# Kernel optimization log

Measured on AMD Instinct MI355X. Metric: run time of the kernel, lower is better.

## Reference

```python
import jax, jax.numpy as jnp
import numpy as np

N_NODES = 50000
N_EDGES = 800000
D_IN = 512
LATENT = [512, 512, 512]
L2_EPS = 1e-12  # torch F.normalize clamp_min


def _gin_layer(x, src, dst, W, b, eps):
    # sum aggregation of neighbor (source) features into destination nodes
    agg = jax.ops.segment_sum(x[src], dst, num_segments=x.shape[0])  # [N, d]
    h = agg + (1.0 + eps) * x
    return jax.nn.relu(h @ W + b)  # Sequential(Linear, ReLU)


def _l2_normalize(x):
    n = jnp.sqrt(jnp.sum(x * x, axis=-1, keepdims=True))
    return x / jnp.maximum(n, L2_EPS)


def setup_inputs() -> dict:
    key = jax.random.key(0)
    ks = jax.random.split(key, 10)
    x = jax.random.normal(ks[0], (N_NODES, D_IN), dtype=jnp.float32)
    edge_index = jax.random.randint(ks[1], (2, N_EDGES), 0, N_NODES, dtype=jnp.int32)
    dims = [D_IN] + LATENT
    inp = {"x": x, "edge_index": edge_index}
    for i in range(3):
        fan_in = dims[i]
        bound = 1.0 / np.sqrt(fan_in)
        inp[f"W{i+1}"] = jax.random.uniform(ks[2 + 2 * i], (dims[i], dims[i + 1]), jnp.float32, -bound, bound)
        inp[f"b{i+1}"] = jax.random.uniform(ks[3 + 2 * i], (dims[i + 1],), jnp.float32, -bound, bound)
        inp[f"eps{i+1}"] = jnp.zeros((), dtype=jnp.float32)  # train_eps=True, init 0
    return inp


def reference(x, edge_index, W1, b1, eps1, W2, b2, eps2, W3, b3, eps3):
    src, dst = edge_index[0], edge_index[1]
    # layers 0..num_layers-2: GINConv -> L2 normalize -> ReLU
    h = _gin_layer(x, src, dst, W1, b1, eps1)
    h = jax.nn.relu(_l2_normalize(h))
    h = _gin_layer(h, src, dst, W2, b2, eps2)
    h = jax.nn.relu(_l2_normalize(h))
    # final layer: raw GINConv output = logits
    logits = _gin_layer(h, src, dst, W3, b3, eps3)
    probs = jax.nn.softmax(logits, axis=-1)
    return (logits, probs)
```

## Files before the change

### kernel.cpp

```cpp
#include <hip/hip_runtime.h>
#include <stdint.h>

#define N_NODES 50000
#define N_EDGES 800000

typedef unsigned int uint32;

__device__ inline float bflo(uint32 u) { return __builtin_bit_cast(float, u << 16); }
__device__ inline float bfhi(uint32 u) { return __builtin_bit_cast(float, u & 0xffff0000u); }
__device__ inline float bf2f(unsigned short h) { return __builtin_bit_cast(float, (uint32)h << 16); }
__device__ inline unsigned short f2bf(float f) {
    uint32 u = __builtin_bit_cast(uint32, f);
    u += 0x7fffu + ((u >> 16) & 1u);
    return (unsigned short)(u >> 16);
}
__device__ inline uint32 pack2(float lo, float hi) {
    return (uint32)f2bf(lo) | ((uint32)f2bf(hi) << 16);
}

__global__ __launch_bounds__(256) void zero_k(int* p, int n) {
    int i = blockIdx.x * 256 + threadIdx.x;
    if (i < n) p[i] = 0;
}

__global__ __launch_bounds__(256) void count_k(const int* __restrict__ ei, int* __restrict__ cnt) {
    int e = blockIdx.x * 256 + threadIdx.x;
    if (e < N_EDGES) atomicAdd(&cnt[ei[N_EDGES + e]], 1);
}

#define NB 196

__global__ __launch_bounds__(256) void blocksum_k(const int* __restrict__ cnt, int* __restrict__ bsum) {
    int i = blockIdx.x * 256 + threadIdx.x;
    int v = (i < N_NODES) ? cnt[i] : 0;
#pragma unroll
    for (int off = 32; off > 0; off >>= 1) v += __shfl_down(v, off);
    __shared__ int sh[4];
    int w = threadIdx.x >> 6, lane = threadIdx.x & 63;
    if (lane == 0) sh[w] = v;
    __syncthreads();
    if (threadIdx.x == 0) bsum[blockIdx.x] = sh[0] + sh[1] + sh[2] + sh[3];
}

__global__ __launch_bounds__(256) void bscan_k(const int* __restrict__ bsum, int* __restrict__ bpre,
                                               int* __restrict__ rowptr) {
    __shared__ int sh[256];
    int t = threadIdx.x;
    int v = (t < NB) ? bsum[t] : 0;
    sh[t] = v;
    __syncthreads();
    for (int d = 1; d < 256; d <<= 1) {
        int u = (t >= d) ? sh[t - d] : 0;
        __syncthreads();
        sh[t] += u;
        __syncthreads();
    }
    if (t < NB) bpre[t] = sh[t] - v;
    if (t == NB - 1) rowptr[N_NODES] = sh[t];
}

__global__ __launch_bounds__(256) void scatter_k(int* __restrict__ cnt, const int* __restrict__ bpre,
                                                 int* __restrict__ rowptr) {
    int b = blockIdx.x, t = threadIdx.x, i = b * 256 + t;
    int w = t >> 6, lane = t & 63;
    int myv = (i < N_NODES) ? cnt[i] : 0;
    int v = myv;
#pragma unroll
    for (int d = 1; d < 64; d <<= 1) {
        int u = __shfl_up(v, d);
        if (lane >= d) v += u;
    }
    __shared__ int wt[4];
    if (lane == 63) wt[w] = v;
    __syncthreads();
    int off = bpre[b];
    for (int k = 0; k < w; k++) off += wt[k];
    int excl = v - myv + off;
    if (i < N_NODES) {
        rowptr[i] = excl;
        cnt[i] = excl;
    }
}

__global__ __launch_bounds__(256) void fill_k(const int* __restrict__ ei, int* __restrict__ cursor,
                                              int* __restrict__ csr) {
    int e = blockIdx.x * 256 + threadIdx.x;
    if (e < N_EDGES) {
        int d = ei[N_EDGES + e];
        int p = atomicAdd(&cursor[d], 1);
        csr[p] = ei[e];
    }
}

__global__ __launch_bounds__(256) void wprep_k(const float* __restrict__ W,
                                               unsigned short* __restrict__ Whi,
                                               unsigned short* __restrict__ Wlo) {
    __shared__ float sh[64][65];
    int bk = (blockIdx.x & 7) * 64;
    int bn = (blockIdx.x >> 3) * 64;
    int t = threadIdx.x;
    int lr = t >> 4;
    int lc4 = (t & 15) * 4;
#pragma unroll
    for (int i = 0; i < 4; i++) {
        int k = lr + i * 16;
        float4 v = *(const float4*)&W[(size_t)(bk + k) * 512 + bn + lc4];
        sh[k][lc4] = v.x; sh[k][lc4 + 1] = v.y; sh[k][lc4 + 2] = v.z; sh[k][lc4 + 3] = v.w;
    }
    __syncthreads();
#pragma unroll
    for (int i = 0; i < 4; i++) {
        int n = lr + i * 16;
        float w0 = sh[lc4][n], w1 = sh[lc4 + 1][n], w2 = sh[lc4 + 2][n], w3 = sh[lc4 + 3][n];
        ushort4 h, l;
        h.x = f2bf(w0); l.x = f2bf(w0 - bf2f(h.x));
        h.y = f2bf(w1); l.y = f2bf(w1 - bf2f(h.y));
        h.z = f2bf(w2); l.z = f2bf(w2 - bf2f(h.z));
        h.w = f2bf(w3); l.w = f2bf(w3 - bf2f(h.w));
        *(ushort4*)&Whi[(size_t)(bn + n) * 512 + bk + lc4] = h;
        *(ushort4*)&Wlo[(size_t)(bn + n) * 512 + bk + lc4] = l;
    }
}

__global__ __launch_bounds__(256) void xconv_k(const float4* __restrict__ x, uint2* __restrict__ xb) {
    int i = blockIdx.x * 256 + threadIdx.x;
    float4 v = x[i];
    uint2 o;
    o.x = pack2(v.x, v.y);
    o.y = pack2(v.z, v.w);
    xb[i] = o;
}

__global__ __launch_bounds__(256) void scale_k(const uint4* __restrict__ in, const float* __restrict__ ss,
                                               uint4* __restrict__ outp) {
    int node = blockIdx.x * 4 + (threadIdx.x >> 6);
    int lane = threadIdx.x & 63;
    float inv = 1.0f / fmaxf(sqrtf(ss[node]), 1e-12f);
    uint4 q = in[(size_t)node * 64 + lane];
    uint4 o;
    o.x = pack2(bflo(q.x) * inv, bfhi(q.x) * inv);
    o.y = pack2(bflo(q.y) * inv, bfhi(q.y) * inv);
    o.z = pack2(bflo(q.z) * inv, bfhi(q.z) * inv);
    o.w = pack2(bflo(q.w) * inv, bfhi(q.w) * inv);
    outp[(size_t)node * 64 + lane] = o;
}

#define ACC8(Q)                                                     \
    a0 += bflo(Q.x); a1 += bfhi(Q.x); a2 += bflo(Q.y); a3 += bfhi(Q.y); \
    a4 += bflo(Q.z); a5 += bfhi(Q.z); a6 += bflo(Q.w); a7 += bfhi(Q.w);

__global__ __launch_bounds__(256) void agg_k(const uint4* __restrict__ xin,
                                             const int* __restrict__ rowptr,
                                             const int* __restrict__ csr,
                                             const float* __restrict__ eps,
                                             uint4* __restrict__ hout) {
    int node = blockIdx.x * 4 + (threadIdx.x >> 6);
    int lane = threadIdx.x & 63;
    int beg = rowptr[node], end = rowptr[node + 1];
    float a0 = 0.f, a1 = 0.f, a2 = 0.f, a3 = 0.f, a4 = 0.f, a5 = 0.f, a6 = 0.f, a7 = 0.f;
    int e = beg;
    for (; e + 8 <= end; e += 8) {
        int s0 = csr[e],     s1 = csr[e + 1], s2 = csr[e + 2], s3 = csr[e + 3];
        int s4 = csr[e + 4], s5 = csr[e + 5], s6 = csr[e + 6], s7 = csr[e + 7];
        uint4 q0 = xin[(size_t)s0 * 64 + lane];
        uint4 q1 = xin[(size_t)s1 * 64 + lane];
        uint4 q2 = xin[(size_t)s2 * 64 + lane];
        uint4 q3 = xin[(size_t)s3 * 64 + lane];
        uint4 q4 = xin[(size_t)s4 * 64 + lane];
        uint4 q5 = xin[(size_t)s5 * 64 + lane];
        uint4 q6 = xin[(size_t)s6 * 64 + lane];
        uint4 q7 = xin[(size_t)s7 * 64 + lane];
        ACC8(q0) ACC8(q1) ACC8(q2) ACC8(q3)
        ACC8(q4) ACC8(q5) ACC8(q6) ACC8(q7)
    }
    for (; e + 4 <= end; e += 4) {
        int s0 = csr[e], s1 = csr[e + 1], s2 = csr[e + 2], s3 = csr[e + 3];
        uint4 q0 = xin[(size_t)s0 * 64 + lane];
        uint4 q1 = xin[(size_t)s1 * 64 + lane];
        uint4 q2 = xin[(size_t)s2 * 64 + lane];
        uint4 q3 = xin[(size_t)s3 * 64 + lane];
        ACC8(q0) ACC8(q1) ACC8(q2) ACC8(q3)
    }
    for (; e < end; ++e) {
        int s0 = csr[e];
        uint4 q0 = xin[(size_t)s0 * 64 + lane];
        ACC8(q0)
    }
    uint4 qs = xin[(size_t)node * 64 + lane];
    float ws = 1.0f + eps[0];
    a0 = fmaf(ws, bflo(qs.x), a0); a1 = fmaf(ws, bfhi(qs.x), a1);
    a2 = fmaf(ws, bflo(qs.y), a2); a3 = fmaf(ws, bfhi(qs.y), a3);
    a4 = fmaf(ws, bflo(qs.z), a4); a5 = fmaf(ws, bfhi(qs.z), a5);
    a6 = fmaf(ws, bflo(qs.w), a6); a7 = fmaf(ws, bfhi(qs.w), a7);
    uint4 o;
    o.x = pack2(a0, a1);
    o.y = pack2(a2, a3);
    o.z = pack2(a4, a5);
    o.w = pack2(a6, a7);
    hout[(size_t)node * 64 + lane] = o;
}

typedef __bf16 bf16x8 __attribute__((ext_vector_type(8)));
typedef float f32x4 __attribute__((ext_vector_type(4)));

__device__ inline void async16(const void* g, void* l) {
    __builtin_amdgcn_global_load_lds((const __attribute__((address_space(1))) void*)g,
                                     (__attribute__((address_space(3))) void*)l, 16, 0, 0);
}

template <bool SPLIT, bool F32OUT, bool NORM>
__global__ __launch_bounds__(256) void gemm_k(const unsigned short* __restrict__ A,
                                              const unsigned short* __restrict__ Whi,
                                              const unsigned short* __restrict__ Wlo,
                                              const float* __restrict__ bias,
                                              unsigned short* __restrict__ outB,
                                              float* __restrict__ outF,
                                              float* __restrict__ ssOut, int M) {
    constexpr int K = 512, N = 512, BK = 32, TM = 128;
    __shared__ unsigned short lds_a[TM * BK];
    __shared__ unsigned short lds_bh[TM * BK];
    __shared__ unsigned short lds_bl[SPLIT ? TM * BK : 16];
    const int t = threadIdx.x;
    const int w = t >> 6, lane = t & 63;
    const int wrow = w >> 1, wcol = w & 1;

    const int nwg = gridDim.x;
    const int qd = nwg >> 3, rd = nwg & 7;
    const int xcd = blockIdx.x & 7, jj = blockIdx.x >> 3;
    const int wg = (xcd < rd ? xcd * (qd + 1) : rd * (qd + 1) + (xcd - rd) * qd) + jj;
    const int m0 = (wg >> 2) * TM;
    const int n0 = (wg & 3) * TM;

    int r0 = w * 16 + (lane >> 2), cc = (lane & 3) * 8;
    int r1 = 64 + r0;
    int am0 = m0 + r0; am0 = am0 < M ? am0 : M - 1;
    int am1 = m0 + r1; am1 = am1 < M ? am1 : M - 1;
    const unsigned short* ag0 = A + (size_t)am0 * K + cc;
    const unsigned short* ag1 = A + (size_t)am1 * K + cc;
    const unsigned short* bh0 = Whi + (size_t)(n0 + r0) * K + cc;
    const unsigned short* bh1 = Whi + (size_t)(n0 + r1) * K + cc;
    const unsigned short* bl0 = Wlo + (size_t)(n0 + r0) * K + cc;
    const unsigned short* bl1 = Wlo + (size_t)(n0 + r1) * K + cc;
    unsigned short* la0 = lds_a + w * 512;
    unsigned short* la1 = lds_a + 2048 + w * 512;
    unsigned short* lh0 = lds_bh + w * 512;
    unsigned short* lh1 = lds_bh + 2048 + w * 512;
    unsigned short* ll0 = lds_bl + w * 512;
    unsigned short* ll1 = lds_bl + 2048 + w * 512;

    f32x4 acc[4][4] = {};
    const int quad = lane >> 4, l15 = lane & 15;
    const int arow = wrow * 64 + l15;
    const int brow = wcol * 64 + l15;

    for (int k0 = 0; k0 < K; k0 += BK) {
        __syncthreads();
        async16(ag0 + k0, la0);
        async16(ag1 + k0, la1);
        async16(bh0 + k0, lh0);
        async16(bh1 + k0, lh1);
        if (SPLIT) {
            async16(bl0 + k0, ll0);
            async16(bl1 + k0, ll1);
        }
        __syncthreads();
        bf16x8 af[4], bh[4], bl[4];
#pragma unroll
        for (int i = 0; i < 4; i++)
            af[i] = *(const bf16x8*)&lds_a[(arow + i * 16) * BK + quad * 8];
#pragma unroll
        for (int j = 0; j < 4; j++)
            bh[j] = *(const bf16x8*)&lds_bh[(brow + j * 16) * BK + quad * 8];
        if (SPLIT) {
#pragma unroll
            for (int j = 0; j < 4; j++)
                bl[j] = *(const bf16x8*)&lds_bl[(brow + j * 16) * BK + quad * 8];
        }
#pragma unroll
        for (int i = 0; i < 4; i++)
#pragma unroll
            for (int j = 0; j < 4; j++) {
                acc[i][j] = __builtin_amdgcn_mfma_f32_16x16x32_bf16(af[i], bh[j], acc[i][j], 0, 0, 0);
                if (SPLIT)
                    acc[i][j] = __builtin_amdgcn_mfma_f32_16x16x32_bf16(af[i], bl[j], acc[i][j], 0, 0, 0);
            }
    }

#pragma unroll
    for (int i = 0; i < 4; i++) {
        int mbase = m0 + wrow * 64 + i * 16 + quad * 4;
        float rs[4] = {0.f, 0.f, 0.f, 0.f};
#pragma unroll
        for (int j = 0; j < 4; j++) {
            int n = n0 + wcol * 64 + j * 16 + l15;
            float bv = bias[n];
#pragma unroll
            for (int r = 0; r < 4; r++) {
                int m = mbase + r;
                if (m < M) {
                    float v = fmaxf(acc[i][j][r] + bv, 0.0f);
                    if (NORM) rs[r] += v * v;
                    if (F32OUT) outF[(size_t)m * N + n] = v;
                    else        outB[(size_t)m * N + n] = f2bf(v);
                }
            }
        }
        if (NORM) {
#pragma unroll
            for (int r = 0; r < 4; r++) {
                float s = rs[r];
                s += __shfl_xor(s, 1);
                s += __shfl_xor(s, 2);
                s += __shfl_xor(s, 4);
                s += __shfl_xor(s, 8);
                int m = mbase + r;
                if (l15 == 0 && m < M) atomicAdd(&ssOut[m], s);
            }
        }
    }
}

__global__ __launch_bounds__(256) void softmax_k(const float* __restrict__ logits,
                                                 float* __restrict__ probs) {
    int node = blockIdx.x * 4 + (threadIdx.x >> 6);
    int lane = threadIdx.x & 63;
    const float4* zp = (const float4*)(logits + (size_t)node * 512);
    float4 q0 = zp[lane * 2], q1 = zp[lane * 2 + 1];
    float f[8] = {q0.x, q0.y, q0.z, q0.w, q1.x, q1.y, q1.z, q1.w};
    float m = f[0];
#pragma unroll
    for (int i = 1; i < 8; i++) m = fmaxf(m, f[i]);
#pragma unroll
    for (int off = 32; off > 0; off >>= 1) m = fmaxf(m, __shfl_xor(m, off));
    float e[8], s = 0.f;
#pragma unroll
    for (int i = 0; i < 8; i++) { e[i] = __expf(f[i] - m); s += e[i]; }
#pragma unroll
    for (int off = 32; off > 0; off >>= 1) s += __shfl_xor(s, off);
    float inv = 1.0f / s;
    float4* pp = (float4*)(probs + (size_t)node * 512);
    pp[lane * 2]     = make_float4(e[0] * inv, e[1] * inv, e[2] * inv, e[3] * inv);
    pp[lane * 2 + 1] = make_float4(e[4] * inv, e[5] * inv, e[6] * inv, e[7] * inv);
}

extern "C" void kernel_launch(void* const* d_in, const int* in_sizes, int n_in,
                              void* d_out, int out_size, void* d_ws, size_t ws_size,
                              hipStream_t stream) {
    (void)in_sizes; (void)n_in; (void)out_size; (void)ws_size;
    const float* x = (const float*)d_in[0];
    const int* ei = (const int*)d_in[1];
    const float* W1 = (const float*)d_in[2];
    const float* b1 = (const float*)d_in[3];
    const float* e1 = (const float*)d_in[4];
    const float* W2 = (const float*)d_in[5];
    const float* b2 = (const float*)d_in[6];
    const float* e2 = (const float*)d_in[7];
    const float* W3 = (const float*)d_in[8];
    const float* b3 = (const float*)d_in[9];
    const float* e3 = (const float*)d_in[10];
    float* out = (float*)d_out;
    float* out_logits = out;
    float* out_probs = out + (size_t)N_NODES * 512;

    char* ws = (char*)d_ws;
    int* rowptr = (int*)ws;
    int* cursor = rowptr + 50048;
    int* csr = cursor + 50048;
    int* bsum = csr + N_EDGES;
    int* bpre = bsum + 256;
    float* ss = (float*)(bpre + 256);
    float* ss1 = ss;
    float* ss2 = ss + 50048;
    unsigned short* Wsp = (unsigned short*)(ss + 2 * 50048);
    unsigned short* f0 = Wsp + 3 * 524288;
    unsigned short* fA = f0 + (size_t)N_NODES * 512;
    unsigned short* f1 = fA + (size_t)N_NODES * 512;
    unsigned short* f2 = f1 + (size_t)N_NODES * 512;

    zero_k<<<196, 256, 0, stream>>>(cursor, N_NODES);
    zero_k<<<392, 256, 0, stream>>>((int*)ss, 2 * 50048);
    count_k<<<(N_EDGES + 255) / 256, 256, 0, stream>>>(ei, cursor);
    blocksum_k<<<NB, 256, 0, stream>>>(cursor, bsum);
    bscan_k<<<1, 256, 0, stream>>>(bsum, bpre, rowptr);
    scatter_k<<<NB, 256, 0, stream>>>(cursor, bpre, rowptr);
    fill_k<<<(N_EDGES + 255) / 256, 256, 0, stream>>>(ei, cursor, csr);

    wprep_k<<<64, 256, 0, stream>>>(W1, Wsp,           Wsp + 262144);
    wprep_k<<<64, 256, 0, stream>>>(W2, Wsp + 524288,  Wsp + 786432);
    wprep_k<<<64, 256, 0, stream>>>(W3, Wsp + 1048576, Wsp + 1310720);

    xconv_k<<<25000, 256, 0, stream>>>((const float4*)x, (uint2*)f0);

    const int GG = 4 * ((N_NODES + 127) / 128);

    agg_k<<<12500, 256, 0, stream>>>((const uint4*)f0, rowptr, csr, e1, (uint4*)fA);
    gemm_k<false, false, true><<<GG, 256, 0, stream>>>(fA, Wsp, Wsp + 262144, b1, f1, nullptr, ss1, N_NODES);
    scale_k<<<12500, 256, 0, stream>>>((const uint4*)f1, ss1, (uint4*)f2);
    agg_k<<<12500, 256, 0, stream>>>((const uint4*)f2, rowptr, csr, e2, (uint4*)fA);
    gemm_k<false, false, true><<<GG, 256, 0, stream>>>(fA, Wsp + 524288, Wsp + 786432, b2, f1, nullptr, ss2, N_NODES);
    scale_k<<<12500, 256, 0, stream>>>((const uint4*)f1, ss2, (uint4*)f2);
    agg_k<<<12500, 256, 0, stream>>>((const uint4*)f2, rowptr, csr, e3, (uint4*)fA);
    gemm_k<true, true, false><<<GG, 256, 0, stream>>>(fA, Wsp + 1048576, Wsp + 1310720, b3, nullptr, out_logits, nullptr, N_NODES);
    softmax_k<<<N_NODES / 4, 256, 0, stream>>>(out_logits, out_probs);
}
```

Baseline: 1.004 ms.

## Fold L2 normalization into aggregation and double-buffer GEMM LDS loads

The separate scale pass that rewrote normalized bf16 features is replaced by a tiny per-node inverse-norm kernel. Aggregation then weights each gathered neighbor row by its inverse norm, which removes a full read and write of the 50000x512 feature tensor per layer. The GEMM main loop is also double-buffered: the next K-slice is loaded asynchronously into a second LDS buffer while MFMAs run on the current one, with one barrier per iteration instead of two. The costs are an extra scalar gather per edge, a change in rounding since features are no longer re-rounded after scaling, doubled LDS usage, and a possible race because only a barrier guards the async LDS loads.

```diff
diff --git a/kernel.cpp b/kernel.cpp
--- a/kernel.cpp
+++ b/kernel.cpp
@@ -131,28 +131,23 @@
     xb[i] = o;
 }
 
-__global__ __launch_bounds__(256) void scale_k(const uint4* __restrict__ in, const float* __restrict__ ss,
-                                               uint4* __restrict__ outp) {
-    int node = blockIdx.x * 4 + (threadIdx.x >> 6);
-    int lane = threadIdx.x & 63;
-    float inv = 1.0f / fmaxf(sqrtf(ss[node]), 1e-12f);
-    uint4 q = in[(size_t)node * 64 + lane];
-    uint4 o;
-    o.x = pack2(bflo(q.x) * inv, bfhi(q.x) * inv);
-    o.y = pack2(bflo(q.y) * inv, bfhi(q.y) * inv);
-    o.z = pack2(bflo(q.z) * inv, bfhi(q.z) * inv);
-    o.w = pack2(bflo(q.w) * inv, bfhi(q.w) * inv);
-    outp[(size_t)node * 64 + lane] = o;
-}
-
-#define ACC8(Q)                                                     \
-    a0 += bflo(Q.x); a1 += bfhi(Q.x); a2 += bflo(Q.y); a3 += bfhi(Q.y); \
-    a4 += bflo(Q.z); a5 += bfhi(Q.z); a6 += bflo(Q.w); a7 += bfhi(Q.w);
-
+__global__ __launch_bounds__(256) void invn_k(const float* __restrict__ ss, float* __restrict__ invn) {
+    int i = blockIdx.x * 256 + threadIdx.x;
+    if (i < N_NODES) invn[i] = 1.0f / fmaxf(sqrtf(ss[i]), 1e-12f);
+}
+
+#define ACCW(Q, W)                                                            \
+    a0 = fmaf(W, bflo(Q.x), a0); a1 = fmaf(W, bfhi(Q.x), a1);                 \
+    a2 = fmaf(W, bflo(Q.y), a2); a3 = fmaf(W, bfhi(Q.y), a3);                 \
+    a4 = fmaf(W, bflo(Q.z), a4); a5 = fmaf(W, bfhi(Q.z), a5);                 \
+    a6 = fmaf(W, bflo(Q.w), a6); a7 = fmaf(W, bfhi(Q.w), a7);
+
+template <bool SCALED>
 __global__ __launch_bounds__(256) void agg_k(const uint4* __restrict__ xin,
                                              const int* __restrict__ rowptr,
                                              const int* __restrict__ csr,
                                              const float* __restrict__ eps,
+                                             const float* __restrict__ invn,
                                              uint4* __restrict__ hout) {
     int node = blockIdx.x * 4 + (threadIdx.x >> 6);
     int lane = threadIdx.x & 63;
@@ -170,28 +165,26 @@
         uint4 q5 = xin[(size_t)s5 * 64 + lane];
         uint4 q6 = xin[(size_t)s6 * 64 + lane];
         uint4 q7 = xin[(size_t)s7 * 64 + lane];
-        ACC8(q0) ACC8(q1) ACC8(q2) ACC8(q3)
-        ACC8(q4) ACC8(q5) ACC8(q6) ACC8(q7)
-    }
-    for (; e + 4 <= end; e += 4) {
-        int s0 = csr[e], s1 = csr[e + 1], s2 = csr[e + 2], s3 = csr[e + 3];
-        uint4 q0 = xin[(size_t)s0 * 64 + lane];
-        uint4 q1 = xin[(size_t)s1 * 64 + lane];
-        uint4 q2 = xin[(size_t)s2 * 64 + lane];
-        uint4 q3 = xin[(size_t)s3 * 64 + lane];
-        ACC8(q0) ACC8(q1) ACC8(q2) ACC8(q3)
+        float w0 = SCALED ? invn[s0] : 1.0f;
+        float w1 = SCALED ? invn[s1] : 1.0f;
+        float w2 = SCALED ? invn[s2] : 1.0f;
+        float w3 = SCALED ? invn[s3] : 1.0f;
+        float w4 = SCALED ? invn[s4] : 1.0f;
+        float w5 = SCALED ? invn[s5] : 1.0f;
+        float w6 = SCALED ? invn[s6] : 1.0f;
+        float w7 = SCALED ? invn[s7] : 1.0f;
+        ACCW(q0, w0) ACCW(q1, w1) ACCW(q2, w2) ACCW(q3, w3)
+        ACCW(q4, w4) ACCW(q5, w5) ACCW(q6, w6) ACCW(q7, w7)
     }
     for (; e < end; ++e) {
         int s0 = csr[e];
         uint4 q0 = xin[(size_t)s0 * 64 + lane];
-        ACC8(q0)
+        float w0 = SCALED ? invn[s0] : 1.0f;
+        ACCW(q0, w0)
     }
     uint4 qs = xin[(size_t)node * 64 + lane];
-    float ws = 1.0f + eps[0];
-    a0 = fmaf(ws, bflo(qs.x), a0); a1 = fmaf(ws, bfhi(qs.x), a1);
-    a2 = fmaf(ws, bflo(qs.y), a2); a3 = fmaf(ws, bfhi(qs.y), a3);
-    a4 = fmaf(ws, bflo(qs.z), a4); a5 = fmaf(ws, bfhi(qs.z), a5);
-    a6 = fmaf(ws, bflo(qs.w), a6); a7 = fmaf(ws, bfhi(qs.w), a7);
+    float wsf = (1.0f + eps[0]) * (SCALED ? invn[node] : 1.0f);
+    ACCW(qs, wsf)
     uint4 o;
     o.x = pack2(a0, a1);
     o.y = pack2(a2, a3);
@@ -216,10 +209,11 @@
                                               unsigned short* __restrict__ outB,
                                               float* __restrict__ outF,
                                               float* __restrict__ ssOut, int M) {
-    constexpr int K = 512, N = 512, BK = 32, TM = 128;
-    __shared__ unsigned short lds_a[TM * BK];
-    __shared__ unsigned short lds_bh[TM * BK];
-    __shared__ unsigned short lds_bl[SPLIT ? TM * BK : 16];
+    constexpr int K = 512, N = 512, BK = 32, TM = 128, NK = K / BK;
+    constexpr int BUF = TM * BK;
+    __shared__ unsigned short lds_a[2 * BUF];
+    __shared__ unsigned short lds_bh[2 * BUF];
+    __shared__ unsigned short lds_bl[SPLIT ? 2 * BUF : 16];
     const int t = threadIdx.x;
     const int w = t >> 6, lane = t & 63;
     const int wrow = w >> 1, wcol = w & 1;
@@ -241,50 +235,63 @@
     const unsigned short* bh1 = Whi + (size_t)(n0 + r1) * K + cc;
     const unsigned short* bl0 = Wlo + (size_t)(n0 + r0) * K + cc;
     const unsigned short* bl1 = Wlo + (size_t)(n0 + r1) * K + cc;
-    unsigned short* la0 = lds_a + w * 512;
-    unsigned short* la1 = lds_a + 2048 + w * 512;
-    unsigned short* lh0 = lds_bh + w * 512;
-    unsigned short* lh1 = lds_bh + 2048 + w * 512;
-    unsigned short* ll0 = lds_bl + w * 512;
-    unsigned short* ll1 = lds_bl + 2048 + w * 512;
+    const int wo = w * 512;
 
     f32x4 acc[4][4] = {};
     const int quad = lane >> 4, l15 = lane & 15;
     const int arow = wrow * 64 + l15;
     const int brow = wcol * 64 + l15;
 
-    for (int k0 = 0; k0 < K; k0 += BK) {
+    auto stage = [&](int k0, int buf) {
+        unsigned short* da = lds_a + buf * BUF + wo;
+        unsigned short* dh = lds_bh + buf * BUF + wo;
+        async16(ag0 + k0, da);
+        async16(ag1 + k0, da + 2048);
+        async16(bh0 + k0, dh);
+        async16(bh1 + k0, dh + 2048);
+        if (SPLIT) {
+            unsigned short* dl = lds_bl + buf * BUF + wo;
+            async16(bl0 + k0, dl);
+            async16(bl1 + k0, dl + 2048);
+        }
+    };
+
+    auto compute = [&](int buf) {
+        const unsigned short* ba = lds_a + buf * BUF;
+        const unsigned short* bb = lds_bh + buf * BUF;
+        bf16x8 af[4], bhf[4], blf[4];
+#pragma unroll
+        for (int i = 0; i < 4; i++)
+            af[i] = *(const bf16x8*)&ba[(arow + i * 16) * BK + quad * 8];
+#pragma unroll
+        for (int j = 0; j < 4; j++)
+            bhf[j] = *(const bf16x8*)&bb[(brow + j * 16) * BK + quad * 8];
+        if (SPLIT) {
+            const unsigned short* bl = lds_bl + buf * BUF;
+#pragma unroll
+            for (int j = 0; j < 4; j++)
+                blf[j] = *(const bf16x8*)&bl[(brow + j * 16) * BK + quad * 8];
+        }
+#pragma unroll
+        for (int i = 0; i < 4; i++)
+#pragma unroll
+            for (int j = 0; j < 4; j++) {
+                acc[i][j] = __builtin_amdgcn_mfma_f32_16x16x32_bf16(af[i], bhf[j], acc[i][j], 0, 0, 0);
+                if (SPLIT)
+                    acc[i][j] = __builtin_amdgcn_mfma_f32_16x16x32_bf16(af[i], blf[j], acc[i][j], 0, 0, 0);
+            }
+    };
+
+    stage(0, 0);
+    __syncthreads();
+    int cur = 0;
+    for (int ks = 0; ks < NK - 1; ++ks) {
+        stage((ks + 1) * BK, cur ^ 1);
+        compute(cur);
         __syncthreads();
-        async16(ag0 + k0, la0);
-        async16(ag1 + k0, la1);
-        async16(bh0 + k0, lh0);
-        async16(bh1 + k0, lh1);
-        if (SPLIT) {
-            async16(bl0 + k0, ll0);
-            async16(bl1 + k0, ll1);
-        }
-        __syncthreads();
-        bf16x8 af[4], bh[4], bl[4];
-#pragma unroll
-        for (int i = 0; i < 4; i++)
-            af[i] = *(const bf16x8*)&lds_a[(arow + i * 16) * BK + quad * 8];
-#pragma unroll
-        for (int j = 0; j < 4; j++)
-            bh[j] = *(const bf16x8*)&lds_bh[(brow + j * 16) * BK + quad * 8];
-        if (SPLIT) {
-#pragma unroll
-            for (int j = 0; j < 4; j++)
-                bl[j] = *(const bf16x8*)&lds_bl[(brow + j * 16) * BK + quad * 8];
-        }
-#pragma unroll
-        for (int i = 0; i < 4; i++)
-#pragma unroll
-            for (int j = 0; j < 4; j++) {
-                acc[i][j] = __builtin_amdgcn_mfma_f32_16x16x32_bf16(af[i], bh[j], acc[i][j], 0, 0, 0);
-                if (SPLIT)
-                    acc[i][j] = __builtin_amdgcn_mfma_f32_16x16x32_bf16(af[i], bl[j], acc[i][j], 0, 0, 0);
-            }
-    }
+        cur ^= 1;
+    }
+    compute(cur);
 
 #pragma unroll
     for (int i = 0; i < 4; i++) {
@@ -368,14 +375,14 @@
     int* csr = cursor + 50048;
     int* bsum = csr + N_EDGES;
     int* bpre = bsum + 256;
-    float* ss = (float*)(bpre + 256);
+    float* invn = (float*)(bpre + 256);
+    float* ss = invn + 50048;
     float* ss1 = ss;
     float* ss2 = ss + 50048;
     unsigned short* Wsp = (unsigned short*)(ss + 2 * 50048);
     unsigned short* f0 = Wsp + 3 * 524288;
     unsigned short* fA = f0 + (size_t)N_NODES * 512;
     unsigned short* f1 = fA + (size_t)N_NODES * 512;
-    unsigned short* f2 = f1 + (size_t)N_NODES * 512;
 
     zero_k<<<196, 256, 0, stream>>>(cursor, N_NODES);
     zero_k<<<392, 256, 0, stream>>>((int*)ss, 2 * 50048);
@@ -393,13 +400,13 @@
 
     const int GG = 4 * ((N_NODES + 127) / 128);
 
-    agg_k<<<12500, 256, 0, stream>>>((const uint4*)f0, rowptr, csr, e1, (uint4*)fA);
+    agg_k<false><<<12500, 256, 0, stream>>>((const uint4*)f0, rowptr, csr, e1, nullptr, (uint4*)fA);
     gemm_k<false, false, true><<<GG, 256, 0, stream>>>(fA, Wsp, Wsp + 262144, b1, f1, nullptr, ss1, N_NODES);
-    scale_k<<<12500, 256, 0, stream>>>((const uint4*)f1, ss1, (uint4*)f2);
-    agg_k<<<12500, 256, 0, stream>>>((const uint4*)f2, rowptr, csr, e2, (uint4*)fA);
+    invn_k<<<196, 256, 0, stream>>>(ss1, invn);
+    agg_k<true><<<12500, 256, 0, stream>>>((const uint4*)f1, rowptr, csr, e2, invn, (uint4*)fA);
     gemm_k<false, false, true><<<GG, 256, 0, stream>>>(fA, Wsp + 524288, Wsp + 786432, b2, f1, nullptr, ss2, N_NODES);
-    scale_k<<<12500, 256, 0, stream>>>((const uint4*)f1, ss2, (uint4*)f2);
-    agg_k<<<12500, 256, 0, stream>>>((const uint4*)f2, rowptr, csr, e3, (uint4*)fA);
+    invn_k<<<196, 256, 0, stream>>>(ss2, invn);
+    agg_k<true><<<12500, 256, 0, stream>>>((const uint4*)f1, rowptr, csr, e3, invn, (uint4*)fA);
     gemm_k<true, true, false><<<GG, 256, 0, stream>>>(fA, Wsp + 1048576, Wsp + 1310720, b3, nullptr, out_logits, nullptr, N_NODES);
     softmax_k<<<N_NODES / 4, 256, 0, stream>>>(out_logits, out_probs);
 }
```

Measured after the change: 989.5 us. No clear change (-1.4%).
